# Optimization experiments

Measured on AMD Instinct MI355X. Metric: run time of the kernel, lower is better.

## Reference

```python
import jax, jax.numpy as jnp
import numpy as np

B, CIN, GC, PL = 4, 256, 64, 64
HL, WL = 128, 128           # low-res x
H, W = 256, 256             # guide resolution
K, DIL = 3, 1               # window_size, dilation
BN_EPS = 1e-5


def setup_inputs() -> dict:
    key = jax.random.key(0)
    k1, k2, k3 = jax.random.split(key, 3)
    return {
        "x": jax.random.normal(k1, (B, CIN, HL, WL), jnp.float32),
        "guide": jax.random.normal(k2, (B, GC, H, W), jnp.float32),
        "W_conv": jax.random.normal(k3, (PL, CIN + GC), jnp.float32) * (1.0 / np.sqrt(CIN + GC)),
        "bn_gamma": jnp.ones((PL,), jnp.float32),
        "bn_beta": jnp.zeros((PL,), jnp.float32),
    }


def _local_attn_2d(q, k, v, ksize, dil):
    # q,k: [B,Cq,H,W]; v: [B,Cv,H,W]; sliding-window attention over ksize x ksize
    Cq = q.shape[1]
    pad = dil * (ksize - 1) // 2
    kp = jnp.pad(k, ((0, 0), (0, 0), (pad, pad), (pad, pad)))
    vp = jnp.pad(v, ((0, 0), (0, 0), (pad, pad), (pad, pad)))
    Hh, Ww = q.shape[2], q.shape[3]
    scores = []
    for i in range(ksize):
        for j in range(ksize):
            kk = kp[:, :, i * dil:i * dil + Hh, j * dil:j * dil + Ww]
            scores.append(jnp.einsum('bchw,bchw->bhw', q, kk))
    s = jnp.stack(scores, axis=1) * (1.0 / np.sqrt(Cq))  # [B,K*K,H,W]
    a = jax.nn.softmax(s, axis=1)
    out = jnp.zeros_like(v)
    idx = 0
    for i in range(ksize):
        for j in range(ksize):
            vv = vp[:, :, i * dil:i * dil + Hh, j * dil:j * dil + Ww]
            out = out + a[:, idx][:, None] * vv
            idx += 1
    return out


def reference(x, guide, W_conv, bn_gamma, bn_beta):
    # UpCatConv1x1: bilinear upsample x to guide res, concat, 1x1 conv (no bias)
    xu = jax.image.resize(x, (x.shape[0], x.shape[1], H, W), method='bilinear')
    cat = jnp.concatenate([xu, guide], axis=1)        # [B, CIN+GC, H, W]
    xv = jnp.einsum('oc,bchw->bohw', W_conv, cat)     # [B, PL, H, W]
    out = _local_attn_2d(guide, guide, xv, K, DIL)
    # BatchNorm2d (training-mode batch statistics)
    mean = jnp.mean(out, axis=(0, 2, 3), keepdims=True)
    var = jnp.var(out, axis=(0, 2, 3), keepdims=True)
    out = (out - mean) * jax.lax.rsqrt(var + BN_EPS)
    out = out * bn_gamma[None, :, None, None] + bn_beta[None, :, None, None]
    return out
```

## Files before the change

kernel.cpp:

```cpp
#include <hip/hip_runtime.h>
#include <math.h>

#define BB 4
#define CIN 256
#define GC 64
#define PL 64
#define HL 128
#define WL 128
#define HH 256
#define WW 256
#define HWLO (HL*WL)
#define HW (HH*WW)
#define NPIX (BB*HW)

typedef __attribute__((ext_vector_type(8))) short bf16x8;
typedef __attribute__((ext_vector_type(4))) float f32x4;

#define XV_OFF 0u
#define Y1_OFF 33554432u
#define STATS_OFF 50331648u
#define PB_OFF 50332672u

static __device__ __forceinline__ unsigned short f2bf(float f) {
    unsigned int u = __float_as_uint(f);
    u = (u + 0x7FFFu + ((u >> 16) & 1u)) >> 16;
    return (unsigned short)u;
}
static __device__ __forceinline__ float bf2f(unsigned short s) {
    return __uint_as_float(((unsigned int)s) << 16);
}

__global__ __launch_bounds__(512) void k_gemm_lo(const float* __restrict__ x,
                                                 const float* __restrict__ Wc,
                                                 float* __restrict__ y1) {
    __shared__ unsigned short lw[64 * 264];
    __shared__ unsigned short la[128 * 40];
    int t = threadIdx.x;
    int b = blockIdx.x >> 7;
    int row = blockIdx.x & 127;
    int lane = t & 63, wid = t >> 6;
    int g = lane >> 4, fr = lane & 15;

    for (int i = t; i < 64 * 256; i += 512) {
        int m = i >> 8, k = i & 255;
        lw[m * 264 + k] = f2bf(Wc[m * 320 + k]);
    }

    f32x4 acc[4];
#pragma unroll
    for (int m = 0; m < 4; ++m) acc[m] = (f32x4){0.f, 0.f, 0.f, 0.f};

    const float* xb = x + (size_t)b * CIN * HWLO + row * WL;
    int px = t & 127, kg = t >> 7;

    for (int kt = 0; kt < 8; ++kt) {
        int k0 = kt * 32;
        short pk[8];
#pragma unroll
        for (int j = 0; j < 8; ++j)
            pk[j] = (short)f2bf(xb[(size_t)(k0 + kg * 8 + j) * HWLO + px]);
        __syncthreads();
        *(bf16x8*)(&la[px * 40 + kg * 8]) = *(bf16x8*)pk;
        __syncthreads();
        bf16x8 bfr = *(const bf16x8*)(&la[(wid * 16 + fr) * 40 + g * 8]);
#pragma unroll
        for (int m = 0; m < 4; ++m) {
            bf16x8 af = *(const bf16x8*)(&lw[(m * 16 + fr) * 264 + k0 + g * 8]);
            acc[m] = __builtin_amdgcn_mfma_f32_16x16x32_bf16(af, bfr, acc[m], 0, 0, 0);
        }
    }

    float* yb = y1 + (size_t)b * 64 * HWLO + row * WL + wid * 16 + fr;
#pragma unroll
    for (int m = 0; m < 4; ++m)
#pragma unroll
        for (int r = 0; r < 4; ++r)
            yb[(size_t)(m * 16 + g * 4 + r) * HWLO] = acc[m][r];
}

__global__ __launch_bounds__(512) void k_conv_hi(const float* __restrict__ guide,
                                                 const float* __restrict__ Wc,
                                                 const float* __restrict__ y1,
                                                 unsigned short* __restrict__ xv) {
    __shared__ unsigned short lg[256 * 72];
    __shared__ unsigned short lw[64 * 72];
    int t = threadIdx.x;
    int bid = blockIdx.x;
    int swz = (bid & 7) * 128 + (bid >> 3);
    int b = swz >> 8, h = swz & 255;
    int lane = t & 63, wid = t >> 6, g = lane >> 4, fr = lane & 15;

    for (int i = t; i < 64 * 64; i += 512) {
        int m = i >> 6, k = i & 63;
        lw[m * 72 + k] = f2bf(Wc[m * 320 + 256 + k]);
    }
    const float* gb = guide + (size_t)b * GC * HW + (size_t)h * WW;
#pragma unroll
    for (int q = 0; q < 4; ++q) {
        int a = t + q * 512;
        int px = a & 255, kg = a >> 8;
        short pk[8];
#pragma unroll
        for (int j = 0; j < 8; ++j)
            pk[j] = (short)f2bf(gb[(size_t)(kg * 8 + j) * HW + px]);
        *(bf16x8*)(&lg[px * 72 + kg * 8]) = *(bf16x8*)pk;
    }
    __syncthreads();

    f32x4 acc[4][2];
#pragma unroll
    for (int m = 0; m < 4; ++m)
#pragma unroll
        for (int n = 0; n < 2; ++n) acc[m][n] = (f32x4){0.f, 0.f, 0.f, 0.f};

#pragma unroll
    for (int kt = 0; kt < 2; ++kt) {
        bf16x8 bfr[2];
#pragma unroll
        for (int n = 0; n < 2; ++n)
            bfr[n] = *(const bf16x8*)(&lg[(wid * 32 + n * 16 + fr) * 72 + kt * 32 + g * 8]);
#pragma unroll
        for (int m = 0; m < 4; ++m) {
            bf16x8 af = *(const bf16x8*)(&lw[(m * 16 + fr) * 72 + kt * 32 + g * 8]);
#pragma unroll
            for (int n = 0; n < 2; ++n)
                acc[m][n] = __builtin_amdgcn_mfma_f32_16x16x32_bf16(af, bfr[n], acc[m][n], 0, 0, 0);
        }
    }
    __syncthreads();

    float* yb = (float*)lg;
    int m0 = h >> 1; int iy0, iy1; float wy0;
    if (h & 1) { iy0 = m0; iy1 = (m0 + 1 < HL) ? m0 + 1 : HL - 1; wy0 = 0.75f; }
    else       { iy0 = (m0 - 1 >= 0) ? m0 - 1 : 0; iy1 = m0;      wy0 = 0.25f; }
    float wy1 = 1.f - wy0;
    const float* y1b = y1 + (size_t)b * 64 * HWLO;
    for (int i = t; i < 64 * 128; i += 512) {
        int ch = i >> 7, ix = i & 127;
        yb[ch * 132 + ix] = wy0 * y1b[(size_t)ch * HWLO + iy0 * WL + ix]
                          + wy1 * y1b[(size_t)ch * HWLO + iy1 * WL + ix];
    }
    __syncthreads();

    int ix0v[2], ix1v[2]; float wx0v[2];
#pragma unroll
    for (int n = 0; n < 2; ++n) {
        int w = wid * 32 + n * 16 + fr;
        int mm = w >> 1;
        if (w & 1) { ix0v[n] = mm; ix1v[n] = (mm + 1 < WL) ? mm + 1 : WL - 1; wx0v[n] = 0.75f; }
        else       { ix0v[n] = (mm - 1 >= 0) ? mm - 1 : 0; ix1v[n] = mm;      wx0v[n] = 0.25f; }
    }
    unsigned short* xb = xv + (size_t)b * 64 * HW + (size_t)h * WW;
#pragma unroll
    for (int m = 0; m < 4; ++m)
#pragma unroll
        for (int n = 0; n < 2; ++n) {
            int w = wid * 32 + n * 16 + fr;
#pragma unroll
            for (int r = 0; r < 4; ++r) {
                int ch = m * 16 + g * 4 + r;
                float up = wx0v[n] * yb[ch * 132 + ix0v[n]]
                         + (1.f - wx0v[n]) * yb[ch * 132 + ix1v[n]];
                xb[(size_t)ch * HW + w] = f2bf(acc[m][n][r] + up);
            }
        }
}

__global__ __launch_bounds__(256) void k_attn(const float* __restrict__ guide,
                                              const unsigned short* __restrict__ xv,
                                              float* __restrict__ out,
                                              float* __restrict__ pb) {
    __shared__ float ls[8][3][264];
    __shared__ float lo[8][256];
    __shared__ float part[64][2];
    int t = threadIdx.x;
    int bid = blockIdx.x;
    int swz = (bid & 7) * 128 + (bid >> 3);
    int b = swz >> 8, h = swz & 255;
    bool rok[3] = { h > 0, true, h < HH - 1 };
    int hr[3] = { h > 0 ? h - 1 : 0, h, h < HH - 1 ? h + 1 : HH - 1 };

    if (t < 48) { int cc = t / 6, rem = t % 6; ls[cc][rem >> 1][(rem & 1) ? 257 : 0] = 0.f; }
    if (t < 128) part[t >> 1][t & 1] = 0.f;

    float s[9];
#pragma unroll
    for (int k = 0; k < 9; ++k) s[k] = 0.f;

    const float* gB = guide + (size_t)b * GC * HW;
    float pf[24];
#pragma unroll
    for (int cc = 0; cc < 8; ++cc)
#pragma unroll
        for (int r = 0; r < 3; ++r)
            pf[cc * 3 + r] = rok[r] ? gB[(size_t)cc * HW + (size_t)hr[r] * WW + t] : 0.f;

    for (int c0 = 0; c0 < GC; c0 += 8) {
        __syncthreads();
#pragma unroll
        for (int cc = 0; cc < 8; ++cc)
#pragma unroll
            for (int r = 0; r < 3; ++r)
                ls[cc][r][1 + t] = pf[cc * 3 + r];
        __syncthreads();
        if (c0 + 8 < GC) {
#pragma unroll
            for (int cc = 0; cc < 8; ++cc)
#pragma unroll
                for (int r = 0; r < 3; ++r)
                    pf[cc * 3 + r] = rok[r] ? gB[(size_t)(c0 + 8 + cc) * HW + (size_t)hr[r] * WW + t] : 0.f;
        }
#pragma unroll
        for (int cc = 0; cc < 8; ++cc) {
            float q = ls[cc][1][1 + t];
#pragma unroll
            for (int r = 0; r < 3; ++r)
#pragma unroll
                for (int dj = 0; dj < 3; ++dj)
                    s[r * 3 + dj] = fmaf(q, ls[cc][r][t + dj], s[r * 3 + dj]);
        }
    }

    float mx = s[0] * 0.125f;
#pragma unroll
    for (int k = 0; k < 9; ++k) { s[k] *= 0.125f; mx = fmaxf(mx, s[k]); }
    float den = 0.f;
#pragma unroll
    for (int k = 0; k < 9; ++k) { s[k] = __expf(s[k] - mx); den += s[k]; }
    float inv = 1.f / den;
#pragma unroll
    for (int k = 0; k < 9; ++k) s[k] *= inv;

    const unsigned short* vB = xv + (size_t)b * 64 * HW;
    float* oB = out + (size_t)b * 64 * HW + (size_t)h * WW + t;
    int rcc = t >> 5, rln = t & 31;

    unsigned short pfu[24];
#pragma unroll
    for (int cc = 0; cc < 8; ++cc)
#pragma unroll
        for (int r = 0; r < 3; ++r)
            pfu[cc * 3 + r] = rok[r] ? vB[(size_t)cc * HW + (size_t)hr[r] * WW + t] : (unsigned short)0;

    for (int c0 = 0; c0 < PL; c0 += 8) {
        __syncthreads();
#pragma unroll
        for (int cc = 0; cc < 8; ++cc)
#pragma unroll
            for (int r = 0; r < 3; ++r)
                ls[cc][r][1 + t] = bf2f(pfu[cc * 3 + r]);
        if (c0 > 0) {
            float sv = 0.f, qv = 0.f;
#pragma unroll
            for (int j = 0; j < 8; ++j) {
                float v = lo[rcc][rln + 32 * j];
                sv += v; qv = fmaf(v, v, qv);
            }
#pragma unroll
            for (int d = 16; d >= 1; d >>= 1) { sv += __shfl_xor(sv, d); qv += __shfl_xor(qv, d); }
            if (rln == 0) { part[c0 - 8 + rcc][0] += sv; part[c0 - 8 + rcc][1] += qv; }
        }
        __syncthreads();
        if (c0 + 8 < PL) {
#pragma unroll
            for (int cc = 0; cc < 8; ++cc)
#pragma unroll
                for (int r = 0; r < 3; ++r)
                    pfu[cc * 3 + r] = rok[r] ? vB[(size_t)(c0 + 8 + cc) * HW + (size_t)hr[r] * WW + t] : (unsigned short)0;
        }
#pragma unroll
        for (int cc = 0; cc < 8; ++cc) {
            float o = 0.f;
#pragma unroll
            for (int r = 0; r < 3; ++r)
#pragma unroll
                for (int dj = 0; dj < 3; ++dj)
                    o = fmaf(s[r * 3 + dj], ls[cc][r][t + dj], o);
            oB[(size_t)(c0 + cc) * HW] = o;
            lo[cc][t] = o;
        }
    }
    __syncthreads();
    {
        float sv = 0.f, qv = 0.f;
#pragma unroll
        for (int j = 0; j < 8; ++j) {
            float v = lo[rcc][rln + 32 * j];
            sv += v; qv = fmaf(v, v, qv);
        }
#pragma unroll
        for (int d = 16; d >= 1; d >>= 1) { sv += __shfl_xor(sv, d); qv += __shfl_xor(qv, d); }
        if (rln == 0) { part[56 + rcc][0] += sv; part[56 + rcc][1] += qv; }
    }
    __syncthreads();
    if (t < 128) pb[(size_t)bid * 128 + (t & 1) * 64 + (t >> 1)] = part[t >> 1][t & 1];
}

__global__ __launch_bounds__(256) void k_reduce(const float* __restrict__ pb,
                                                float* __restrict__ stats) {
    int c = blockIdx.x;
    float acc = 0.f;
#pragma unroll
    for (int i = 0; i < 4; ++i)
        acc += pb[(size_t)(threadIdx.x + i * 256) * 128 + c];
#pragma unroll
    for (int d = 32; d >= 1; d >>= 1) acc += __shfl_xor(acc, d);
    __shared__ float lred[4];
    if ((threadIdx.x & 63) == 0) lred[threadIdx.x >> 6] = acc;
    __syncthreads();
    if (threadIdx.x == 0) stats[c] = lred[0] + lred[1] + lred[2] + lred[3];
}

__global__ __launch_bounds__(256) void k_norm(float* __restrict__ out,
                                              const float* __restrict__ stats,
                                              const float* __restrict__ gamma,
                                              const float* __restrict__ beta) {
    size_t idx = (size_t)blockIdx.x * 256 + threadIdx.x;
    int c = (int)((idx >> 14) & (PL - 1));
    float4 v = ((const float4*)out)[idx];
    float n = (float)NPIX;
    float mean = stats[c] / n;
    float var = stats[PL + c] / n - mean * mean;
    float sc = gamma[c] * rsqrtf(var + 1e-5f);
    float bs = beta[c] - mean * sc;
    v.x = fmaf(v.x, sc, bs);
    v.y = fmaf(v.y, sc, bs);
    v.z = fmaf(v.z, sc, bs);
    v.w = fmaf(v.w, sc, bs);
    ((float4*)out)[idx] = v;
}

extern "C" void kernel_launch(void* const* d_in, const int* in_sizes, int n_in,
                              void* d_out, int out_size, void* d_ws, size_t ws_size,
                              hipStream_t stream) {
    const float* x     = (const float*)d_in[0];
    const float* guide = (const float*)d_in[1];
    const float* Wc    = (const float*)d_in[2];
    const float* gamma = (const float*)d_in[3];
    const float* beta  = (const float*)d_in[4];
    float* out = (float*)d_out;

    char* ws = (char*)d_ws;
    unsigned short* xvb = (unsigned short*)(ws + XV_OFF);
    float* y1    = (float*)(ws + Y1_OFF);
    float* stats = (float*)(ws + STATS_OFF);
    float* pb    = (float*)(ws + PB_OFF);

    k_gemm_lo<<<512, 512, 0, stream>>>(x, Wc, y1);
    k_conv_hi<<<1024, 512, 0, stream>>>(guide, Wc, y1, xvb);
    k_attn<<<1024, 256, 0, stream>>>(guide, xvb, out, pb);
    k_reduce<<<128, 256, 0, stream>>>(pb, stats);
    k_norm<<<(NPIX * PL) / (256 * 4), 256, 0, stream>>>(out, stats, gamma, beta);
}
```

Measured before the change: 256.9 us.

## Store attention output as bf16, fuse stat reduction via atomics, prefetch gemm loads

The attention kernel now writes its pre-normalization output as bf16 into a workspace buffer instead of fp32 into the final output. The normalization pass reads that bf16 buffer and writes fp32, which cuts the intermediate traffic. Per-block BN partial sums are accumulated with atomicAdd into stats zeroed by a memset, so the separate reduce kernel goes away. The low-res GEMM also prefetches the next K-slice of x during the MFMA work. The cost is bf16 rounding of the output before normalization and nondeterministic atomic summation order. OB_OFF aliases the Y1 workspace region, which is safe only because y1 is consumed by k_conv_hi before k_attn writes obuf.

```diff
diff --git a/kernel.cpp b/kernel.cpp
--- a/kernel.cpp
+++ b/kernel.cpp
@@ -18,8 +18,8 @@
 
 #define XV_OFF 0u
 #define Y1_OFF 33554432u
-#define STATS_OFF 50331648u
-#define PB_OFF 50332672u
+#define OB_OFF 33554432u
+#define STATS_OFF 67108864u
 
 static __device__ __forceinline__ unsigned short f2bf(float f) {
     unsigned int u = __float_as_uint(f);
@@ -53,15 +53,21 @@
     const float* xb = x + (size_t)b * CIN * HWLO + row * WL;
     int px = t & 127, kg = t >> 7;
 
+    short pk[8];
+#pragma unroll
+    for (int j = 0; j < 8; ++j)
+        pk[j] = (short)f2bf(xb[(size_t)(kg * 8 + j) * HWLO + px]);
+
     for (int kt = 0; kt < 8; ++kt) {
         int k0 = kt * 32;
-        short pk[8];
-#pragma unroll
-        for (int j = 0; j < 8; ++j)
-            pk[j] = (short)f2bf(xb[(size_t)(k0 + kg * 8 + j) * HWLO + px]);
         __syncthreads();
         *(bf16x8*)(&la[px * 40 + kg * 8]) = *(bf16x8*)pk;
         __syncthreads();
+        if (kt < 7) {
+#pragma unroll
+            for (int j = 0; j < 8; ++j)
+                pk[j] = (short)f2bf(xb[(size_t)(k0 + 32 + kg * 8 + j) * HWLO + px]);
+        }
         bf16x8 bfr = *(const bf16x8*)(&la[(wid * 16 + fr) * 40 + g * 8]);
 #pragma unroll
         for (int m = 0; m < 4; ++m) {
@@ -168,8 +174,8 @@
 
 __global__ __launch_bounds__(256) void k_attn(const float* __restrict__ guide,
                                               const unsigned short* __restrict__ xv,
-                                              float* __restrict__ out,
-                                              float* __restrict__ pb) {
+                                              unsigned short* __restrict__ obuf,
+                                              float* __restrict__ stats) {
     __shared__ float ls[8][3][264];
     __shared__ float lo[8][256];
     __shared__ float part[64][2];
@@ -232,7 +238,7 @@
     for (int k = 0; k < 9; ++k) s[k] *= inv;
 
     const unsigned short* vB = xv + (size_t)b * 64 * HW;
-    float* oB = out + (size_t)b * 64 * HW + (size_t)h * WW + t;
+    unsigned short* oB = obuf + (size_t)b * 64 * HW + (size_t)h * WW + t;
     int rcc = t >> 5, rln = t & 31;
 
     unsigned short pfu[24];
@@ -276,8 +282,10 @@
 #pragma unroll
                 for (int dj = 0; dj < 3; ++dj)
                     o = fmaf(s[r * 3 + dj], ls[cc][r][t + dj], o);
-            oB[(size_t)(c0 + cc) * HW] = o;
-            lo[cc][t] = o;
+            unsigned short ob = f2bf(o);
+            float orv = bf2f(ob);
+            oB[(size_t)(c0 + cc) * HW] = ob;
+            lo[cc][t] = orv;
         }
     }
     __syncthreads();
@@ -293,41 +301,33 @@
         if (rln == 0) { part[56 + rcc][0] += sv; part[56 + rcc][1] += qv; }
     }
     __syncthreads();
-    if (t < 128) pb[(size_t)bid * 128 + (t & 1) * 64 + (t >> 1)] = part[t >> 1][t & 1];
-}
-
-__global__ __launch_bounds__(256) void k_reduce(const float* __restrict__ pb,
-                                                float* __restrict__ stats) {
-    int c = blockIdx.x;
-    float acc = 0.f;
-#pragma unroll
-    for (int i = 0; i < 4; ++i)
-        acc += pb[(size_t)(threadIdx.x + i * 256) * 128 + c];
-#pragma unroll
-    for (int d = 32; d >= 1; d >>= 1) acc += __shfl_xor(acc, d);
-    __shared__ float lred[4];
-    if ((threadIdx.x & 63) == 0) lred[threadIdx.x >> 6] = acc;
-    __syncthreads();
-    if (threadIdx.x == 0) stats[c] = lred[0] + lred[1] + lred[2] + lred[3];
-}
-
-__global__ __launch_bounds__(256) void k_norm(float* __restrict__ out,
+    if (t < 128) atomicAdd(&stats[(t & 1) * 64 + (t >> 1)], part[t >> 1][t & 1]);
+}
+
+__global__ __launch_bounds__(256) void k_norm(const unsigned short* __restrict__ obuf,
                                               const float* __restrict__ stats,
                                               const float* __restrict__ gamma,
-                                              const float* __restrict__ beta) {
-    size_t idx = (size_t)blockIdx.x * 256 + threadIdx.x;
-    int c = (int)((idx >> 14) & (PL - 1));
-    float4 v = ((const float4*)out)[idx];
+                                              const float* __restrict__ beta,
+                                              float* __restrict__ out) {
+    size_t idx8 = (size_t)blockIdx.x * 256 + threadIdx.x;
+    int c = (int)((idx8 >> 13) & 63);
     float n = (float)NPIX;
     float mean = stats[c] / n;
-    float var = stats[PL + c] / n - mean * mean;
+    float var = stats[64 + c] / n - mean * mean;
     float sc = gamma[c] * rsqrtf(var + 1e-5f);
     float bs = beta[c] - mean * sc;
-    v.x = fmaf(v.x, sc, bs);
-    v.y = fmaf(v.y, sc, bs);
-    v.z = fmaf(v.z, sc, bs);
-    v.w = fmaf(v.w, sc, bs);
-    ((float4*)out)[idx] = v;
+    bf16x8 v = ((const bf16x8*)obuf)[idx8];
+    float4 o0, o1;
+    o0.x = fmaf(bf2f((unsigned short)v[0]), sc, bs);
+    o0.y = fmaf(bf2f((unsigned short)v[1]), sc, bs);
+    o0.z = fmaf(bf2f((unsigned short)v[2]), sc, bs);
+    o0.w = fmaf(bf2f((unsigned short)v[3]), sc, bs);
+    o1.x = fmaf(bf2f((unsigned short)v[4]), sc, bs);
+    o1.y = fmaf(bf2f((unsigned short)v[5]), sc, bs);
+    o1.z = fmaf(bf2f((unsigned short)v[6]), sc, bs);
+    o1.w = fmaf(bf2f((unsigned short)v[7]), sc, bs);
+    ((float4*)out)[idx8 * 2]     = o0;
+    ((float4*)out)[idx8 * 2 + 1] = o1;
 }
 
 extern "C" void kernel_launch(void* const* d_in, const int* in_sizes, int n_in,
@@ -341,14 +341,14 @@
     float* out = (float*)d_out;
 
     char* ws = (char*)d_ws;
-    unsigned short* xvb = (unsigned short*)(ws + XV_OFF);
-    float* y1    = (float*)(ws + Y1_OFF);
-    float* stats = (float*)(ws + STATS_OFF);
-    float* pb    = (float*)(ws + PB_OFF);
-
+    unsigned short* xvb  = (unsigned short*)(ws + XV_OFF);
+    float* y1            = (float*)(ws + Y1_OFF);
+    unsigned short* obuf = (unsigned short*)(ws + OB_OFF);
+    float* stats         = (float*)(ws + STATS_OFF);
+
+    hipMemsetAsync(stats, 0, 128 * sizeof(float), stream);
     k_gemm_lo<<<512, 512, 0, stream>>>(x, Wc, y1);
     k_conv_hi<<<1024, 512, 0, stream>>>(guide, Wc, y1, xvb);
-    k_attn<<<1024, 256, 0, stream>>>(guide, xvb, out, pb);
-    k_reduce<<<128, 256, 0, stream>>>(pb, stats);
-    k_norm<<<(NPIX * PL) / (256 * 4), 256, 0, stream>>>(out, stats, gamma, beta);
-}
+    k_attn<<<1024, 256, 0, stream>>>(guide, xvb, obuf, stats);
+    k_norm<<<(NPIX * PL) / (256 * 8), 256, 0, stream>>>(obuf, stats, gamma, beta, out);
+}
```

New measurement: 263.4 us. 2.5% more time.
